# Optimization experiments

Measured on AMD Instinct MI355X. Metric: run time of the kernel, lower is better.

## Reference

```python
import jax, jax.numpy as jnp
import numpy as np

EMBED_DIM = 512
NUM_HEADS = 8
HEAD_DIM = EMBED_DIM // NUM_HEADS
EDGE_DIM = 16
B, N = 2, 2048


def setup_inputs() -> dict:
    key = jax.random.key(0)
    ks = jax.random.split(key, 16)
    s = 1.0 / np.sqrt(EMBED_DIM)
    inp = {
        "x": jax.random.normal(ks[0], (B, N, EMBED_DIM), dtype=jnp.float32),
        "adjacency": jax.random.uniform(ks[1], (B, N, N), dtype=jnp.float32),
        # torch.nn.Linear stores weight as (out, in); we keep that convention
        "Wq": jax.random.uniform(ks[2], (EMBED_DIM, EMBED_DIM), minval=-s, maxval=s),
        "bq": jax.random.uniform(ks[3], (EMBED_DIM,), minval=-s, maxval=s),
        "Wk": jax.random.uniform(ks[4], (EMBED_DIM, EMBED_DIM), minval=-s, maxval=s),
        "bk": jax.random.uniform(ks[5], (EMBED_DIM,), minval=-s, maxval=s),
        "Wv": jax.random.uniform(ks[6], (EMBED_DIM, EMBED_DIM), minval=-s, maxval=s),
        "bv": jax.random.uniform(ks[7], (EMBED_DIM,), minval=-s, maxval=s),
        "Wo": jax.random.uniform(ks[8], (EMBED_DIM, EMBED_DIM), minval=-s, maxval=s),
        "bo": jax.random.uniform(ks[9], (EMBED_DIM,), minval=-s, maxval=s),
        # edge MLP: Linear(1 -> edge_dim) then Linear(edge_dim -> num_heads)
        "We1": jax.random.uniform(ks[10], (EDGE_DIM, 1), minval=-1.0, maxval=1.0),
        "be1": jax.random.uniform(ks[11], (EDGE_DIM,), minval=-1.0, maxval=1.0),
        "We2": jax.random.uniform(ks[12], (NUM_HEADS, EDGE_DIM), minval=-0.25, maxval=0.25),
        "be2": jax.random.uniform(ks[13], (NUM_HEADS,), minval=-0.25, maxval=0.25),
        "edge_bias": jnp.zeros((NUM_HEADS,), dtype=jnp.float32),
    }
    return inp


def reference(x, adjacency, Wq, bq, Wk, bk, Wv, bv, Wo, bo, We1, be1, We2, be2, edge_bias):
    b, n, _ = x.shape
    scale = HEAD_DIM ** (-0.5)

    def split_heads(t):  # (b, n, E) -> (b, H, n, d)
        return t.reshape(b, n, NUM_HEADS, HEAD_DIM).transpose(0, 2, 1, 3)

    q = split_heads(x @ Wq.T + bq)
    k = split_heads(x @ Wk.T + bk)
    v = split_heads(x @ Wv.T + bv)

    # (b, H, n, n)
    attn_scores = jnp.einsum('bhid,bhjd->bhij', q, k) * scale

    # edge MLP applied pointwise to each adjacency entry: 1 -> edge_dim -> num_heads
    # hidden: (b, n, n, edge_dim)
    hidden = jax.nn.relu(adjacency[..., None] * We1[:, 0] + be1)
    edge_attn = jnp.einsum('bijE,hE->bhij', hidden, We2) + be2[None, :, None, None]

    boost = adjacency[:, None, :, :] * edge_bias[None, :, None, None]
    attn_scores = attn_scores + edge_attn + boost

    attn_probs = jax.nn.softmax(attn_scores, axis=-1)
    out = jnp.einsum('bhij,bhjd->bhid', attn_probs, v)
    out = out.transpose(0, 2, 1, 3).reshape(b, n, EMBED_DIM)
    out = out @ Wo.T + bo
    return out
```

## Files before the change

### kernel.cpp

```cpp
#include <hip/hip_runtime.h>
#include <stdint.h>


#define SEQ 2048
#define EMB 512
#define NH  8
#define HD  64
#define NB  2
#define L2E 1.4426950408889634f

typedef unsigned int   u32;
typedef unsigned short u16;
typedef u32   u32x4  __attribute__((ext_vector_type(4)));
typedef float f32x4  __attribute__((ext_vector_type(4)));
typedef __bf16 bf16x8 __attribute__((ext_vector_type(8)));
typedef _Float16 f16x4 __attribute__((ext_vector_type(4)));

#define MFMA16(a, b, c) __builtin_amdgcn_mfma_f32_16x16x32_bf16((a), (b), (c), 0, 0, 0)

static __device__ __forceinline__ u16 f2bf(float f) {
  return __builtin_bit_cast(u16, (__bf16)f);
}
static __device__ __forceinline__ u32 pack2(float a, float b) {
  return (u32)f2bf(a) | ((u32)f2bf(b) << 16);
}
static __device__ __forceinline__ u16 f2h(float f) {
  return __builtin_bit_cast(u16, (_Float16)f);
}
static __device__ __forceinline__ bf16x8 ldfrag(const u16* p) {
  return __builtin_bit_cast(bf16x8, *(const u32x4*)p);
}
static __device__ __forceinline__ void glds16(const u16* g, u16* l) {
  __builtin_amdgcn_global_load_lds(
      (const __attribute__((address_space(1))) u32*)(const void*)g,
      (__attribute__((address_space(3))) u32*)(void*)l, 16, 0, 0);
}


__global__ void prep_kernel(const float* __restrict__ x, const float* __restrict__ adj,
                            const float* __restrict__ Wq, const float* __restrict__ Wk,
                            const float* __restrict__ Wv, const float* __restrict__ Wo,
                            const float* __restrict__ We1, const float* __restrict__ be1,
                            const float* __restrict__ We2, const float* __restrict__ be2,
                            const float* __restrict__ ebias,
                            u16* __restrict__ xb, u16* __restrict__ wqkv,
                            u16* __restrict__ wob, float* __restrict__ co,
                            u16* __restrict__ at) {
  __shared__ float Ts[16 * 72];
  const int blk = blockIdx.x, tid = threadIdx.x;
  if (blk < 2048) {
    int i = (blk * 256 + tid) * 4;
    float4 v = *(const float4*)(x + i);
    *(uint2*)(xb + i) = make_uint2(pack2(v.x, v.y), pack2(v.z, v.w));
  } else if (blk < 3072) {
    int i = ((blk - 2048) * 256 + tid) * 4;
    int m = i >> 18;
    int off = i & 262143;
    const float* src = (m == 0) ? Wq : ((m == 1) ? Wk : ((m == 2) ? Wv : Wo));
    u16* dst = (m < 3) ? (wqkv + (size_t)m * 262144) : wob;
    float4 v = *(const float4*)(src + off);
    *(uint2*)(dst + off) = make_uint2(pack2(v.x, v.y), pack2(v.z, v.w));
  } else if (blk == 3072) {
    const int e = tid & 15, h = tid >> 4;
    if (tid < 128) {
      co[49 + e * 8 + h] = 0.0f;
      if (h == 0) { co[17 + e] = 0.0f; co[33 + e] = 0.0f; }
    }
    __syncthreads();
    if (tid < 128) {
      float w1 = We1[e], b1 = be1[e], w2 = We2[h * 16 + e];
      float u0 = b1, u1 = w1 + b1;
      bool on  = (u0 >= 0.0f) && (u1 >= 0.0f);
      bool off = (u0 <= 0.0f) && (u1 <= 0.0f);
      bool crossing = (!on) && (!off);
      float ca = on ? (w2 * b1) : (crossing ? 0.5f * w2 * b1 : 0.0f);
      float cb = on ? (w2 * w1) : (crossing ? 0.5f * w2 * w1 : 0.0f);
      #pragma unroll
      for (int d = 1; d < 16; d <<= 1) { ca += __shfl_xor(ca, d); cb += __shfl_xor(cb, d); }
      if (e == 0) { co[h] = (be2[h] + ca) * L2E; co[8 + h] = (ebias[h] + cb) * L2E; }
      unsigned long long msk = __ballot(crossing);
      int midx = __popcll(msk & 0xFFFFull & ((1ull << e) - 1ull));
      int mcnt = __popcll(msk & 0xFFFFull);
      if (crossing) {
        co[49 + midx * 8 + h] = 0.5f * w2 * L2E;
        if (h == 0) { co[17 + midx] = w1; co[33 + midx] = b1; }
      }
      if (tid == 0) ((int*)co)[16] = mcnt;
    }
  } else {
    const int blk2 = blk - 3073;
    const int b = blk2 >> 7, it16 = blk2 & 127;
    const float* src = adj + ((size_t)b * SEQ + it16 * 16) * SEQ;
    u16* dst = at + (size_t)b * 4194304 + (size_t)it16 * 32768;
    const int row = tid >> 4, jl = tid & 15;
    const int jq = tid >> 4, il = tid & 15;
    for (int jc = 0; jc < SEQ; jc += 64) {
      float4 v = *(const float4*)(src + (size_t)row * SEQ + jc + jl * 4);
      __syncthreads();
      *(float4*)&Ts[row * 72 + jl * 4] = v;
      __syncthreads();
      float a0 = Ts[il * 72 + jq * 4 + 0];
      float a1 = Ts[il * 72 + jq * 4 + 1];
      float a2 = Ts[il * 72 + jq * 4 + 2];
      float a3 = Ts[il * 72 + jq * 4 + 3];
      uint2 w2v = make_uint2((u32)f2h(a0) | ((u32)f2h(a1) << 16),
                             (u32)f2h(a2) | ((u32)f2h(a3) << 16));
      *(uint2*)(dst + (((jc >> 2) + jq) << 6) + il * 4) = w2v;
    }
  }
}

#define LDA 40
__global__ __launch_bounds__(256) void gemm_qkv_kernel(
    const u16* __restrict__ A, const u16* __restrict__ Bm,
    const float* __restrict__ bq, const float* __restrict__ bk, const float* __restrict__ bv,
    u16* __restrict__ qh, u16* __restrict__ ksw, u16* __restrict__ vsw)
{
  __shared__ u16 sm[64 * LDA + 128 * LDA];
  u16* As = sm;
  u16* Bs = sm + 64 * LDA;
  const int tid = threadIdx.x;
  const int lane = tid & 63, w = tid >> 6;
  const int q = lane >> 4, l15 = lane & 15;
  const int m0 = blockIdx.y * 64;
  const int n0 = blockIdx.x * 128;

  f32x4 acc[4][2];
  f32x4 zero = {0.f, 0.f, 0.f, 0.f};
  #pragma unroll
  for (int i = 0; i < 4; i++) { acc[i][0] = zero; acc[i][1] = zero; }

  const bool isA = tid < 128;
  const int arow_ = tid >> 1, ahalf = tid & 1;
  const int brow = tid - 128;
  const u16* ga = A  + (size_t)(m0 + arow_) * EMB + ahalf * 16;
  const u16* gb = Bm + (size_t)(n0 + brow) * EMB;
  u16* la = &As[arow_ * LDA + ahalf * 16];
  u16* lb = &Bs[brow * LDA];

  u32x4 p0, p1, p2, p3;
  if (isA) {
    p0 = *(const u32x4*)(ga); p1 = *(const u32x4*)(ga + 8); ga += 32;
  } else {
    p0 = *(const u32x4*)(gb);      p1 = *(const u32x4*)(gb + 8);
    p2 = *(const u32x4*)(gb + 16); p3 = *(const u32x4*)(gb + 24); gb += 32;
  }

  for (int k0 = 0; k0 < EMB; k0 += 32) {
    __syncthreads();
    if (isA) { *(u32x4*)(la) = p0; *(u32x4*)(la + 8) = p1; }
    else {
      *(u32x4*)(lb)      = p0; *(u32x4*)(lb + 8)  = p1;
      *(u32x4*)(lb + 16) = p2; *(u32x4*)(lb + 24) = p3;
    }
    __syncthreads();
    if (k0 + 32 < EMB) {
      if (isA) { p0 = *(const u32x4*)(ga); p1 = *(const u32x4*)(ga + 8); ga += 32; }
      else {
        p0 = *(const u32x4*)(gb);      p1 = *(const u32x4*)(gb + 8);
        p2 = *(const u32x4*)(gb + 16); p3 = *(const u32x4*)(gb + 24); gb += 32;
      }
    }
    bf16x8 af[4], bfr[2];
    #pragma unroll
    for (int mi = 0; mi < 4; mi++)
      af[mi] = ldfrag(&As[(mi*16 + l15) * LDA + q*8]);
    #pragma unroll
    for (int ni = 0; ni < 2; ni++)
      bfr[ni] = ldfrag(&Bs[(w*32 + ni*16 + l15) * LDA + q*8]);
    #pragma unroll
    for (int mi = 0; mi < 4; mi++)
      #pragma unroll
      for (int ni = 0; ni < 2; ni++)
        acc[mi][ni] = MFMA16(af[mi], bfr[ni], acc[mi][ni]);
  }

  const int mat = n0 >> 9;
  const float* bias = (mat == 0) ? bq : ((mat == 1) ? bk : bv);
  const float mul = (mat == 0) ? 0.125f * L2E : 1.0f;
  const int b_ = m0 >> 11;
  const int nbase = m0 & 2047;

  #pragma unroll
  for (int p = 0; p < 2; p++) {
    __syncthreads();
    if ((w >> 1) == p) {
      #pragma unroll
      for (int ni = 0; ni < 2; ni++) {
        const int dd = (w & 1) * 32 + ni * 16 + l15;
        const float bsv = bias[(n0 & 511) + (w * 32 + ni * 16 + l15)];
        #pragma unroll
        for (int mi = 0; mi < 4; mi++) {
          #pragma unroll
          for (int r = 0; r < 4; r++) {
            const int nr = mi * 16 + q * 4 + r;
            const float val = (acc[mi][ni][r] + bsv) * mul;
            int idx;
            if (mat == 0)      idx = nr * 64 + dd;
            else if (mat == 1) idx = (nr >> 4) * 1024 + ((dd >> 5) << 9)
                                   + ((((dd >> 3) & 3) * 16 + (nr & 15)) << 3) + (dd & 7);
            else               idx = ((dd >> 4) << 10) + (((nr >> 5) & 1) << 9)
                                   + ((((nr >> 3) & 3) * 16 + (dd & 15)) << 3) + (nr & 7);
            sm[idx] = f2bf(val);
          }
        }
      }
    }
    __syncthreads();
    const int hh = ((n0 & 511) >> 6) + p;
    u16* gdst;
    if (mat == 0)      gdst = qh  + ((size_t)(b_ * NH + hh) * SEQ + nbase) * HD;
    else if (mat == 1) gdst = ksw + (size_t)(b_ * NH + hh) * 131072 + (nbase >> 4) * 1024;
    else               gdst = vsw + (size_t)(b_ * NH + hh) * 131072 + (nbase >> 6) * 4096;
    *(u32x4*)(gdst + tid * 16)     = *(const u32x4*)(sm + tid * 16);
    *(u32x4*)(gdst + tid * 16 + 8) = *(const u32x4*)(sm + tid * 16 + 8);
  }
}

__global__ __launch_bounds__(256) void gemm_out_kernel(
    const u16* __restrict__ A, const u16* __restrict__ Bm,
    const float* __restrict__ bo, float* __restrict__ out)
{
  __shared__ u16 As[64 * LDA];
  __shared__ u16 Bs[64 * LDA];
  const int tid = threadIdx.x;
  const int lane = tid & 63, w = tid >> 6;
  const int q = lane >> 4, l15 = lane & 15;
  const int m0 = blockIdx.y * 64;
  const int n0 = blockIdx.x * 64;

  f32x4 acc[4];
  f32x4 zero = {0.f, 0.f, 0.f, 0.f};
  #pragma unroll
  for (int i = 0; i < 4; i++) acc[i] = zero;

  const bool isA = tid < 128;
  const int row = isA ? (tid >> 1) : ((tid - 128) >> 1);
  const int half = tid & 1;
  const u16* g = (isA ? A + (size_t)(m0 + row) * EMB : Bm + (size_t)(n0 + row) * EMB)
               + half * 16;
  u16* l = (isA ? &As[row * LDA] : &Bs[row * LDA]) + half * 16;

  u32x4 p0 = *(const u32x4*)(g);
  u32x4 p1 = *(const u32x4*)(g + 8);
  g += 32;

  for (int k0 = 0; k0 < EMB; k0 += 32) {
    __syncthreads();
    *(u32x4*)(l) = p0; *(u32x4*)(l + 8) = p1;
    __syncthreads();
    if (k0 + 32 < EMB) {
      p0 = *(const u32x4*)(g); p1 = *(const u32x4*)(g + 8); g += 32;
    }
    bf16x8 af[4], bfr;
    #pragma unroll
    for (int mi = 0; mi < 4; mi++)
      af[mi] = ldfrag(&As[(mi*16 + l15) * LDA + q*8]);
    bfr = ldfrag(&Bs[(w*16 + l15) * LDA + q*8]);
    #pragma unroll
    for (int mi = 0; mi < 4; mi++)
      acc[mi] = MFMA16(af[mi], bfr, acc[mi]);
  }

  int col = n0 + w*16 + l15;
  float bsv = bo[col];
  #pragma unroll
  for (int mi = 0; mi < 4; mi++) {
    int rowb = m0 + mi*16 + q*4;
    #pragma unroll
    for (int r = 0; r < 4; r++)
      out[(size_t)(rowb + r) * EMB + col] = acc[mi][r] + bsv;
  }
}

template<int MT>
struct FlashCtx {
  const u16 *kgp, *vgp;
  const u16* aq;
  bf16x8 qf0, qf1;
  float Ah, Bh;
  float ctr[MT], dtr[MT], wtr[MT];
  int lane, w, q, l15;
};

template<int MT>
static __device__ __forceinline__ void flash_stage(const FlashCtx<MT>& c,
                                                   u16* Kb, u16* Vb, int it) {
  const int o = c.w * 1024 + c.lane * 8;
  const u16* kg = c.kgp + it * 4096;
  const u16* vg = c.vgp + it * 4096;
  glds16(kg + o,       Kb + o);
  glds16(kg + o + 512, Kb + o + 512);
  glds16(vg + o,       Vb + o);
  glds16(vg + o + 512, Vb + o + 512);
}

template<int MT>
static __device__ __forceinline__ void flash_iter(
    const FlashCtx<MT>& c, int it, u16* Kb, u16* Vb, u16* nKb, u16* nVb,
    u16* psw, uint2* avc, uint2* avn, f32x4* O, float& lsum)
{
  __syncthreads();
  if (it + 1 < 32) flash_stage(c, nKb, nVb, it + 1);
  const int nx = (it + 1 < 32) ? it + 1 : 31;
  #pragma unroll
  for (int jt = 0; jt < 4; jt++)
    avn[jt] = *(const uint2*)(c.aq + ((nx * 16 + jt * 4) << 6));
  __builtin_amdgcn_sched_barrier(0);

  f32x4 zero = {0.f, 0.f, 0.f, 0.f};
  const int lo = c.lane * 8;

  f32x4 S[4];
  #pragma unroll
  for (int jt = 0; jt < 4; jt++) {
    bf16x8 kf0 = ldfrag(Kb + jt * 1024 + lo);
    bf16x8 kf1 = ldfrag(Kb + jt * 1024 + 512 + lo);
    f32x4 s = MFMA16(kf0, c.qf0, zero);
    S[jt] = MFMA16(kf1, c.qf1, s);
  }

  #pragma unroll
  for (int half = 0; half < 2; half++) {
    #pragma unroll
    for (int jj = 0; jj < 2; jj++) {
      const int jt = half * 2 + jj;
      f16x4 hv = __builtin_bit_cast(f16x4, avc[jt]);
      float p[4];
      #pragma unroll
      for (int r = 0; r < 4; r++) {
        float a = (float)hv[r];
        float e = fmaf(a, c.Bh, c.Ah);
        #pragma unroll
        for (int t = 0; t < MT; t++)
          e = fmaf(fabsf(fmaf(a, c.ctr[t], c.dtr[t])), c.wtr[t], e);
        p[r] = __builtin_amdgcn_exp2f(S[jt][r] + e);
        lsum += p[r];
      }
      *(uint2*)(psw + c.l15 * 72 + jt * 16 + c.q * 4) =
          make_uint2(pack2(p[0], p[1]), pack2(p[2], p[3]));
    }
    bf16x8 pf = ldfrag(psw + c.l15 * 72 + half * 32 + c.q * 8);
    #pragma unroll
    for (int dt = 0; dt < 4; dt++) {
      bf16x8 vf = ldfrag(Vb + dt * 1024 + half * 512 + lo);
      O[dt] = MFMA16(vf, pf, O[dt]);
    }
  }
}

template<int MT>
__device__ __forceinline__ void flash_body(
    u16* Kb0, u16* Kb1, u16* Vb0, u16* Vb1, u16* Pb,
    const u16* __restrict__ qh, const u16* __restrict__ ksw, const u16* __restrict__ vsw,
    const u16* __restrict__ at, const float* __restrict__ coeff, u16* __restrict__ om)
{
  const int tid = threadIdx.x, lane = tid & 63, w = tid >> 6;
  const int q = lane >> 4, l15 = lane & 15;
  const int i0 = blockIdx.x * 64;
  const int h = blockIdx.y, b = blockIdx.z;
  const int bh = b * NH + h;
  const int iw = i0 + w * 16;

  FlashCtx<MT> c;
  c.lane = lane; c.w = w; c.q = q; c.l15 = l15;
  c.Ah = coeff[h]; c.Bh = coeff[8 + h];
  #pragma unroll
  for (int t = 0; t < MT; t++) {
    c.ctr[t] = coeff[17 + t];
    c.dtr[t] = coeff[33 + t];
    c.wtr[t] = coeff[49 + t * 8 + h];
  }
  const u16* qrow = qh + ((size_t)bh * SEQ + iw + l15) * HD;
  c.qf0 = ldfrag(qrow + q * 8);
  c.qf1 = ldfrag(qrow + 32 + q * 8);
  c.kgp = ksw + (size_t)bh * 131072;
  c.vgp = vsw + (size_t)bh * 131072;
  c.aq  = at + (size_t)b * 4194304 + (size_t)(iw >> 4) * 32768 + q * 64 + l15 * 4;

  f32x4 O[4];
  f32x4 zero = {0.f, 0.f, 0.f, 0.f};
  #pragma unroll
  for (int dt = 0; dt < 4; dt++) O[dt] = zero;
  float lsum = 0.0f;

  u16* psw = Pb + w * 1152;

  flash_stage(c, Kb0, Vb0, 0);
  uint2 avA[4], avB[4];
  #pragma unroll
  for (int jt = 0; jt < 4; jt++)
    avA[jt] = *(const uint2*)(c.aq + ((jt * 4) << 6));

  #pragma unroll 1
  for (int it2 = 0; it2 < 32; it2 += 2) {
    flash_iter(c, it2,     Kb0, Vb0, Kb1, Vb1, psw, avA, avB, O, lsum);
    flash_iter(c, it2 + 1, Kb1, Vb1, Kb0, Vb0, psw, avB, avA, O, lsum);
  }

  lsum += __shfl_xor(lsum, 16);
  lsum += __shfl_xor(lsum, 32);
  float rl = 1.0f / lsum;

  u16* orow = om + ((size_t)b * SEQ + iw + l15) * EMB + h * HD + q * 4;
  #pragma unroll
  for (int dt = 0; dt < 4; dt++) {
    float v0 = O[dt][0] * rl, v1 = O[dt][1] * rl;
    float v2 = O[dt][2] * rl, v3 = O[dt][3] * rl;
    *(uint2*)(orow + dt * 16) = make_uint2(pack2(v0, v1), pack2(v2, v3));
  }
}

__global__ __launch_bounds__(256, 3) void flash_kernel(
    const u16* __restrict__ qh, const u16* __restrict__ ksw, const u16* __restrict__ vsw,
    const u16* __restrict__ at, const float* __restrict__ coeff, u16* __restrict__ om)
{
  __shared__ __align__(16) u16 Kb[2][4096];
  __shared__ __align__(16) u16 Vb[2][4096];
  __shared__ __align__(16) u16 Pb[4608];
  const int mt = ((const int*)coeff)[16];
  if (mt <= 4)
    flash_body<4>(Kb[0], Kb[1], Vb[0], Vb[1], Pb, qh, ksw, vsw, at, coeff, om);
  else if (mt <= 8)
    flash_body<8>(Kb[0], Kb[1], Vb[0], Vb[1], Pb, qh, ksw, vsw, at, coeff, om);
  else
    flash_body<16>(Kb[0], Kb[1], Vb[0], Vb[1], Pb, qh, ksw, vsw, at, coeff, om);
}

extern "C" void kernel_launch(void* const* d_in, const int* in_sizes, int n_in,
                              void* d_out, int out_size, void* d_ws, size_t ws_size,
                              hipStream_t stream) {
  const float* x     = (const float*)d_in[0];
  const float* adj   = (const float*)d_in[1];
  const float* Wq    = (const float*)d_in[2];
  const float* bq    = (const float*)d_in[3];
  const float* Wk    = (const float*)d_in[4];
  const float* bk    = (const float*)d_in[5];
  const float* Wv    = (const float*)d_in[6];
  const float* bv    = (const float*)d_in[7];
  const float* Wo    = (const float*)d_in[8];
  const float* bo    = (const float*)d_in[9];
  const float* We1   = (const float*)d_in[10];
  const float* be1   = (const float*)d_in[11];
  const float* We2   = (const float*)d_in[12];
  const float* be2   = (const float*)d_in[13];
  const float* ebias = (const float*)d_in[14];
  float* out = (float*)d_out;

  char* ws = (char*)d_ws;
  u16*   xb   = (u16*)(ws + 0);
  u16*   wqkv = (u16*)(ws + 4194304);
  u16*   wob  = (u16*)(ws + 5767168);
  u16*   qh   = (u16*)(ws + 6291456);
  u16*   ksw  = (u16*)(ws + 10485760);
  u16*   vsw  = (u16*)(ws + 14680064);
  u16*   om   = (u16*)(ws + 18874368);
  float* co   = (float*)(ws + 23068672);
  u16*   at   = (u16*)(ws + 23072768);
  if (ws_size < 39849984) return;

  prep_kernel<<<3329, 256, 0, stream>>>(x, adj, Wq, Wk, Wv, Wo, We1, be1, We2, be2,
                                        ebias, xb, wqkv, wob, co, at);
  gemm_qkv_kernel<<<dim3(12, 64), 256, 0, stream>>>(xb, wqkv, bq, bk, bv, qh, ksw, vsw);
  flash_kernel<<<dim3(32, NH, NB), 256, 0, stream>>>(qh, ksw, vsw, at, co, om);
  gemm_out_kernel<<<dim3(8, 64), 256, 0, stream>>>(om, wob, bo, out);
}
```

Measured before the change: 214.4 us.

## Software-pipeline QK^T one tile ahead in flash loop; widen adjacency transpose blocks

The flash attention loop now computes the QK^T scores for the next key tile while the edge-bias/exp work and PV MFMAs of the current tile run, with K staged two tiles ahead and V one tile ahead. This lets MFMA work overlap the VALU-heavy exponent and edge computation. Separately, the adjacency transpose in the prep kernel is split across 8x more blocks, each handling a 16x256 slab with a single barrier instead of a 32-step loop with two barriers per step. The costs are extra registers for the second score buffer, which may hurt occupancy, and a larger shared-memory tile in prep.

```diff
diff --git a/kernel.cpp b/kernel.cpp
--- a/kernel.cpp
+++ b/kernel.cpp
@@ -46,7 +46,7 @@
                             u16* __restrict__ xb, u16* __restrict__ wqkv,
                             u16* __restrict__ wob, float* __restrict__ co,
                             u16* __restrict__ at) {
-  __shared__ float Ts[16 * 72];
+  __shared__ float Ts[16 * 257];
   const int blk = blockIdx.x, tid = threadIdx.x;
   if (blk < 2048) {
     int i = (blk * 256 + tid) * 4;
@@ -89,23 +89,28 @@
     }
   } else {
     const int blk2 = blk - 3073;
-    const int b = blk2 >> 7, it16 = blk2 & 127;
-    const float* src = adj + ((size_t)b * SEQ + it16 * 16) * SEQ;
-    u16* dst = at + (size_t)b * 4194304 + (size_t)it16 * 32768;
+    const int b = blk2 >> 10, rem = blk2 & 1023;
+    const int it16 = rem >> 3, jc = (rem & 7) * 256;
+    const float* src = adj + ((size_t)b * SEQ + it16 * 16) * SEQ + jc;
+    u16* dst = at + (size_t)b * 4194304 + (size_t)it16 * 32768 + ((size_t)jc >> 2) * 64;
     const int row = tid >> 4, jl = tid & 15;
-    const int jq = tid >> 4, il = tid & 15;
-    for (int jc = 0; jc < SEQ; jc += 64) {
-      float4 v = *(const float4*)(src + (size_t)row * SEQ + jc + jl * 4);
-      __syncthreads();
-      *(float4*)&Ts[row * 72 + jl * 4] = v;
-      __syncthreads();
-      float a0 = Ts[il * 72 + jq * 4 + 0];
-      float a1 = Ts[il * 72 + jq * 4 + 1];
-      float a2 = Ts[il * 72 + jq * 4 + 2];
-      float a3 = Ts[il * 72 + jq * 4 + 3];
-      uint2 w2v = make_uint2((u32)f2h(a0) | ((u32)f2h(a1) << 16),
-                             (u32)f2h(a2) | ((u32)f2h(a3) << 16));
-      *(uint2*)(dst + (((jc >> 2) + jq) << 6) + il * 4) = w2v;
+    #pragma unroll
+    for (int p = 0; p < 4; p++) {
+      float4 v = *(const float4*)(src + (size_t)row * SEQ + p * 64 + jl * 4);
+      *(float4*)&Ts[row * 257 + p * 64 + jl * 4] = v;
+    }
+    __syncthreads();
+    const int il = tid & 15;
+    #pragma unroll
+    for (int wv = 0; wv < 4; wv++) {
+      const int jql = wv * 16 + (tid >> 4);
+      float a0 = Ts[il * 257 + jql * 4 + 0];
+      float a1 = Ts[il * 257 + jql * 4 + 1];
+      float a2 = Ts[il * 257 + jql * 4 + 2];
+      float a3 = Ts[il * 257 + jql * 4 + 3];
+      *(uint2*)(dst + jql * 64 + il * 4) =
+          make_uint2((u32)f2h(a0) | ((u32)f2h(a1) << 16),
+                     (u32)f2h(a2) | ((u32)f2h(a3) << 16));
     }
   }
 }
@@ -284,67 +289,88 @@
 };
 
 template<int MT>
-static __device__ __forceinline__ void flash_stage(const FlashCtx<MT>& c,
-                                                   u16* Kb, u16* Vb, int it) {
+static __device__ __forceinline__ void stageK(const FlashCtx<MT>& c, u16* Kb, int it) {
   const int o = c.w * 1024 + c.lane * 8;
   const u16* kg = c.kgp + it * 4096;
-  const u16* vg = c.vgp + it * 4096;
   glds16(kg + o,       Kb + o);
   glds16(kg + o + 512, Kb + o + 512);
+}
+template<int MT>
+static __device__ __forceinline__ void stageV(const FlashCtx<MT>& c, u16* Vb, int it) {
+  const int o = c.w * 1024 + c.lane * 8;
+  const u16* vg = c.vgp + it * 4096;
   glds16(vg + o,       Vb + o);
   glds16(vg + o + 512, Vb + o + 512);
 }
 
 template<int MT>
+static __device__ __forceinline__ void edge_exp_P(
+    const FlashCtx<MT>& c, const f32x4* S, const uint2* avc, int jt,
+    u16* psw, float& lsum)
+{
+  f16x4 hv = __builtin_bit_cast(f16x4, avc[jt]);
+  float p[4];
+  #pragma unroll
+  for (int r = 0; r < 4; r++) {
+    float a = (float)hv[r];
+    float e = fmaf(a, c.Bh, c.Ah);
+    #pragma unroll
+    for (int t = 0; t < MT; t++)
+      e = fmaf(fabsf(fmaf(a, c.ctr[t], c.dtr[t])), c.wtr[t], e);
+    p[r] = __builtin_amdgcn_exp2f(S[jt][r] + e);
+    lsum += p[r];
+  }
+  *(uint2*)(psw + c.l15 * 72 + jt * 16 + c.q * 4) =
+      make_uint2(pack2(p[0], p[1]), pack2(p[2], p[3]));
+}
+
+template<int MT>
 static __device__ __forceinline__ void flash_iter(
-    const FlashCtx<MT>& c, int it, u16* Kb, u16* Vb, u16* nKb, u16* nVb,
-    u16* psw, uint2* avc, uint2* avn, f32x4* O, float& lsum)
+    const FlashCtx<MT>& c, int t, u16* Kcur, u16* Knext, u16* Vcur, u16* Vnext,
+    u16* psw, uint2* avc, uint2* avn, f32x4* Scur, f32x4* Snew, f32x4* O, float& lsum)
 {
   __syncthreads();
-  if (it + 1 < 32) flash_stage(c, nKb, nVb, it + 1);
-  const int nx = (it + 1 < 32) ? it + 1 : 31;
+  if (t + 2 < 32) stageK(c, Kcur, t + 2);
+  if (t + 1 < 32) stageV(c, Vnext, t + 1);
+  const int nx = (t + 1 < 32) ? t + 1 : 31;
   #pragma unroll
   for (int jt = 0; jt < 4; jt++)
     avn[jt] = *(const uint2*)(c.aq + ((nx * 16 + jt * 4) << 6));
   __builtin_amdgcn_sched_barrier(0);
 
+  const int lo = c.lane * 8;
   f32x4 zero = {0.f, 0.f, 0.f, 0.f};
-  const int lo = c.lane * 8;
-
-  f32x4 S[4];
-  #pragma unroll
-  for (int jt = 0; jt < 4; jt++) {
-    bf16x8 kf0 = ldfrag(Kb + jt * 1024 + lo);
-    bf16x8 kf1 = ldfrag(Kb + jt * 1024 + 512 + lo);
-    f32x4 s = MFMA16(kf0, c.qf0, zero);
-    S[jt] = MFMA16(kf1, c.qf1, s);
-  }
-
-  #pragma unroll
-  for (int half = 0; half < 2; half++) {
-    #pragma unroll
-    for (int jj = 0; jj < 2; jj++) {
-      const int jt = half * 2 + jj;
-      f16x4 hv = __builtin_bit_cast(f16x4, avc[jt]);
-      float p[4];
-      #pragma unroll
-      for (int r = 0; r < 4; r++) {
-        float a = (float)hv[r];
-        float e = fmaf(a, c.Bh, c.Ah);
-        #pragma unroll
-        for (int t = 0; t < MT; t++)
-          e = fmaf(fabsf(fmaf(a, c.ctr[t], c.dtr[t])), c.wtr[t], e);
-        p[r] = __builtin_amdgcn_exp2f(S[jt][r] + e);
-        lsum += p[r];
-      }
-      *(uint2*)(psw + c.l15 * 72 + jt * 16 + c.q * 4) =
-          make_uint2(pack2(p[0], p[1]), pack2(p[2], p[3]));
-    }
-    bf16x8 pf = ldfrag(psw + c.l15 * 72 + half * 32 + c.q * 8);
+
+  edge_exp_P(c, Scur, avc, 0, psw, lsum);
+  edge_exp_P(c, Scur, avc, 1, psw, lsum);
+
+  if (t < 31) {
+    #pragma unroll
+    for (int jt = 0; jt < 4; jt++) {
+      bf16x8 kf0 = ldfrag(Knext + jt * 1024 + lo);
+      bf16x8 kf1 = ldfrag(Knext + jt * 1024 + 512 + lo);
+      f32x4 s = MFMA16(kf0, c.qf0, zero);
+      Snew[jt] = MFMA16(kf1, c.qf1, s);
+    }
+  }
+
+  {
+    bf16x8 pf0 = ldfrag(psw + c.l15 * 72 + c.q * 8);
     #pragma unroll
     for (int dt = 0; dt < 4; dt++) {
-      bf16x8 vf = ldfrag(Vb + dt * 1024 + half * 512 + lo);
-      O[dt] = MFMA16(vf, pf, O[dt]);
+      bf16x8 vf = ldfrag(Vcur + dt * 1024 + lo);
+      O[dt] = MFMA16(vf, pf0, O[dt]);
+    }
+  }
+
+  edge_exp_P(c, Scur, avc, 2, psw, lsum);
+  edge_exp_P(c, Scur, avc, 3, psw, lsum);
+  {
+    bf16x8 pf1 = ldfrag(psw + c.l15 * 72 + 32 + c.q * 8);
+    #pragma unroll
+    for (int dt = 0; dt < 4; dt++) {
+      bf16x8 vf = ldfrag(Vcur + dt * 1024 + 512 + lo);
+      O[dt] = MFMA16(vf, pf1, O[dt]);
     }
   }
 }
@@ -386,16 +412,30 @@
 
   u16* psw = Pb + w * 1152;
 
-  flash_stage(c, Kb0, Vb0, 0);
+  stageK(c, Kb0, 0);
+  stageV(c, Vb0, 0);
+  stageK(c, Kb1, 1);
   uint2 avA[4], avB[4];
   #pragma unroll
   for (int jt = 0; jt < 4; jt++)
     avA[jt] = *(const uint2*)(c.aq + ((jt * 4) << 6));
+  __syncthreads();
+  f32x4 SA[4], SB[4];
+  {
+    const int lo = lane * 8;
+    #pragma unroll
+    for (int jt = 0; jt < 4; jt++) {
+      bf16x8 kf0 = ldfrag(Kb0 + jt * 1024 + lo);
+      bf16x8 kf1 = ldfrag(Kb0 + jt * 1024 + 512 + lo);
+      f32x4 s = MFMA16(kf0, c.qf0, zero);
+      SA[jt] = MFMA16(kf1, c.qf1, s);
+    }
+  }
 
   #pragma unroll 1
-  for (int it2 = 0; it2 < 32; it2 += 2) {
-    flash_iter(c, it2,     Kb0, Vb0, Kb1, Vb1, psw, avA, avB, O, lsum);
-    flash_iter(c, it2 + 1, Kb1, Vb1, Kb0, Vb0, psw, avB, avA, O, lsum);
+  for (int t2 = 0; t2 < 32; t2 += 2) {
+    flash_iter(c, t2,     Kb0, Kb1, Vb0, Vb1, psw, avA, avB, SA, SB, O, lsum);
+    flash_iter(c, t2 + 1, Kb1, Kb0, Vb1, Vb0, psw, avB, avA, SB, SA, O, lsum);
   }
 
   lsum += __shfl_xor(lsum, 16);
@@ -459,7 +499,7 @@
   u16*   at   = (u16*)(ws + 23072768);
   if (ws_size < 39849984) return;
 
-  prep_kernel<<<3329, 256, 0, stream>>>(x, adj, Wq, Wk, Wv, Wo, We1, be1, We2, be2,
+  prep_kernel<<<5121, 256, 0, stream>>>(x, adj, Wq, Wk, Wv, Wo, We1, be1, We2, be2,
                                         ebias, xb, wqkv, wob, co, at);
   gemm_qkv_kernel<<<dim3(12, 64), 256, 0, stream>>>(xb, wqkv, bq, bk, bv, qh, ksw, vsw);
   flash_kernel<<<dim3(32, NH, NB), 256, 0, stream>>>(qh, ksw, vsw, at, co, om);
```

Measured after the change: 193.4 us. 9.8% less time.
